# Kernel optimization log

Hardware: AMD Instinct MI355X
Metric: run time of the kernel (lower is better)

## Reference

```python
import jax, jax.numpy as jnp
import numpy as np

N_NODES = 100000
N_EDGES = 1600000
D_IN = 64
D_OUT = 64
ALPHA = 0.5


def setup_inputs() -> dict:
    key = jax.random.key(0)
    k_x, k_ei, k_w, k_ws, k_bs, k_wd, k_bd = jax.random.split(key, 7)
    x = jax.random.normal(k_x, (N_NODES, D_IN), dtype=jnp.float32)
    edge_index = jax.random.randint(k_ei, (2, N_EDGES), 0, N_NODES, dtype=jnp.int64)
    edge_weight = jax.random.uniform(k_w, (N_EDGES,), dtype=jnp.float32)
    # torch Linear init: uniform(-1/sqrt(fan_in), 1/sqrt(fan_in))
    bound = 1.0 / np.sqrt(D_IN)
    W_src = jax.random.uniform(k_ws, (D_OUT, D_IN), minval=-bound, maxval=bound, dtype=jnp.float32)
    b_src = jax.random.uniform(k_bs, (D_OUT,), minval=-bound, maxval=bound, dtype=jnp.float32)
    W_dst = jax.random.uniform(k_wd, (D_OUT, D_IN), minval=-bound, maxval=bound, dtype=jnp.float32)
    b_dst = jax.random.uniform(k_bd, (D_OUT,), minval=-bound, maxval=bound, dtype=jnp.float32)
    return {"x": x, "edge_index": edge_index, "edge_weight": edge_weight,
            "W_src": W_src, "b_src": b_src, "W_dst": W_dst, "b_dst": b_dst}


def _dir_norm_spmm(row, col, w, x, n):
    """Compute (D_out^{-1/2} A D_in^{-1/2}) @ x for A with entries (row, col, w)."""
    out_deg = jax.ops.segment_sum(w, row, num_segments=n)  # row sums (dim=1)
    in_deg = jax.ops.segment_sum(w, col, num_segments=n)   # col sums (dim=0)
    d_out = jnp.where(out_deg > 0, out_deg ** -0.5, 0.0)
    d_in = jnp.where(in_deg > 0, in_deg ** -0.5, 0.0)
    w_norm = w * d_out[row] * d_in[col]                    # [E]
    # SpMM: out[i] = sum_{e: row_e = i} w_norm_e * x[col_e]
    return jax.ops.segment_sum(w_norm[:, None] * x[col], row, num_segments=n)


def reference(x, edge_index, edge_weight, W_src, b_src, W_dst, b_dst):
    row, col = edge_index[0], edge_index[1]
    n = x.shape[0]
    agg_fwd = _dir_norm_spmm(row, col, edge_weight, x, n)   # adj_norm @ x
    agg_bwd = _dir_norm_spmm(col, row, edge_weight, x, n)   # adj_t_norm @ x
    out = ALPHA * (agg_fwd @ W_src.T + b_src) + (1.0 - ALPHA) * (agg_bwd @ W_dst.T + b_dst)
    return out
```

## Files before the change

### kernel.cpp

```cpp
#include <hip/hip_runtime.h>

#define D 64
#define ALPHA 0.5f
#define FXSCALE 16777216.f
#define CE 2048
#define BSH 9
#define BN 512

typedef unsigned long long u64;
typedef unsigned short u16;
typedef unsigned int u32;
typedef float f32x4 __attribute__((ext_vector_type(4)));

static __device__ __forceinline__ u16 f2bf(float f) {
    unsigned u = __float_as_uint(f);
    unsigned r = (u + 0x7fffu + ((u >> 16) & 1u)) >> 16;
    return (u16)r;
}
static __device__ __forceinline__ float bf2f(u16 h) {
    return __uint_as_float(((unsigned)h) << 16);
}
static __device__ __forceinline__ float dinv_of_fx(u32 fx) {
    float s = (float)fx * (1.f / FXSCALE);
    return (s > 0.f) ? rsqrtf(s) : 0.f;
}

__global__ void p1_hist_kernel(const int* __restrict__ row, const int* __restrict__ col,
                               int* __restrict__ bh, int N, int E, int NCH, int NBUCK) {
    __shared__ u32 h[512];
    int t = threadIdx.x, ch = blockIdx.x;
    h[t] = 0;
    __syncthreads();
    int e0 = ch * CE, e1 = min(E, e0 + CE);
    for (int e = e0 + t; e < e1; e += 512) {
        atomicAdd(&h[(u32)row[e] >> BSH], 1u);
        atomicAdd(&h[(u32)(N + col[e]) >> BSH], 1u);
    }
    __syncthreads();
    for (int b = t; b < NBUCK; b += 512)
        bh[(size_t)b * NCH + ch] = (int)h[b];
}

__global__ void scan1i_kernel(const int* __restrict__ src, int* __restrict__ bsum, int SZ) {
    __shared__ int s[512];
    int t = threadIdx.x;
    int i = blockIdx.x * 512 + t;
    s[t] = (i < SZ) ? src[i] : 0;
    __syncthreads();
    for (int off = 256; off; off >>= 1) {
        if (t < off) s[t] += s[t + off];
        __syncthreads();
    }
    if (t == 0) bsum[blockIdx.x] = s[0];
}

__global__ void scan2w_kernel(int* __restrict__ bsum, int nb) {
    __shared__ int s[1024];
    int t = threadIdx.x;
    int v = (t < nb) ? bsum[t] : 0;
    s[t] = v;
    __syncthreads();
    for (int off = 1; off < 1024; off <<= 1) {
        int u = (t >= off) ? s[t - off] : 0;
        __syncthreads();
        s[t] += u;
        __syncthreads();
    }
    if (t < nb) bsum[t] = s[t] - v;
}

__global__ void scan3i_kernel(const int* __restrict__ src, const int* __restrict__ bsum,
                              int* __restrict__ dst, int SZ) {
    __shared__ int s[512];
    int t = threadIdx.x;
    int i = blockIdx.x * 512 + t;
    int v = (i < SZ) ? src[i] : 0;
    s[t] = v;
    __syncthreads();
    for (int off = 1; off < 512; off <<= 1) {
        int u = (t >= off) ? s[t - off] : 0;
        __syncthreads();
        s[t] += u;
        __syncthreads();
    }
    if (i < SZ) dst[i] = bsum[blockIdx.x] + s[t] - v;
}

__global__ __launch_bounds__(512)
void p3_transform_kernel(const int* __restrict__ row, const int* __restrict__ col,
                         const float* __restrict__ w, const int* __restrict__ scanned,
                         u64* __restrict__ ent,
                         const float* __restrict__ x,
                         const float* __restrict__ Ws, const float* __restrict__ Wd,
                         u16* __restrict__ y1, u16* __restrict__ y2,
                         int N, int E, int NCH, int NBUCK, int NT, int total_blocks) {
    __shared__ u64 smem[6432];
    int b = blockIdx.x;
    int t = threadIdx.x;
    int t_before = (int)(((long long)b * NT) / total_blocks);
    bool is_t = (int)(((long long)(b + 1) * NT) / total_blocks) > t_before;

    if (!is_t) {
        int ch = b - t_before;
        u64* ebuf   = smem;
        u16* ebkt   = (u16*)(smem + 4096);
        u32* hc     = (u32*)(smem + 5120);
        u32* hstart = (u32*)(smem + 5376);
        u32* hoff   = (u32*)(smem + 5632);
        int* s      = (int*)(smem + 5888);
        hc[t] = 0;
        __syncthreads();
        int e0 = ch * CE, e1 = min(E, e0 + CE);
        for (int e = e0 + t; e < e1; e += 512) {
            atomicAdd(&hc[(u32)row[e] >> BSH], 1u);
            atomicAdd(&hc[(u32)(N + col[e]) >> BSH], 1u);
        }
        __syncthreads();
        int v = (int)hc[t];
        s[t] = v;
        __syncthreads();
        for (int off = 1; off < 512; off <<= 1) {
            int u = (t >= off) ? s[t - off] : 0;
            __syncthreads();
            s[t] += u;
            __syncthreads();
        }
        hstart[t] = (u32)(s[t] - v);
        hoff[t]   = (u32)(s[t] - v);
        hc[t] = (t < NBUCK) ? (u32)scanned[(size_t)t * NCH + ch] : 0u;
        __syncthreads();
        for (int e = e0 + t; e < e1; e += 512) {
            int r = row[e], c = col[e];
            u32 wb = __float_as_uint(w[e]);
            u32 b1 = (u32)r >> BSH;
            u64 q1 = ((u64)wb << 32) | ((u32)c << BSH) | ((u32)r & (BN - 1));
            u32 p1 = atomicAdd(&hoff[b1], 1u);
            ebuf[p1] = q1; ebkt[p1] = (u16)b1;
            u32 d2 = (u32)(N + c);
            u32 b2 = d2 >> BSH;
            u64 q2 = ((u64)wb << 32) | ((u32)r << BSH) | (d2 & (BN - 1));
            u32 p2 = atomicAdd(&hoff[b2], 1u);
            ebuf[p2] = q2; ebkt[p2] = (u16)b2;
        }
        __syncthreads();
        int nent = 2 * (e1 - e0);
        for (int p = t; p < nent; p += 512) {
            u32 bb = ebkt[p];
            ent[(size_t)hc[bb] + (u32)p - hstart[bb]] = ebuf[p];
        }
        return;
    }

    float* xs  = (float*)smem;
    float* Wt1 = xs + 64 * 65;
    float* Wt2 = Wt1 + 64 * 68;
    for (int i = t; i < 4096; i += 512) {
        int o = i >> 6, k = i & 63;
        Wt1[k * 68 + o] = Ws[i];
        Wt2[k * 68 + o] = Wd[i];
    }
    int r0 = t_before * 64;
    for (int i = t; i < 4096; i += 512) {
        int r = i >> 6, k = i & 63;
        int gr = r0 + r;
        xs[r * 65 + k] = (gr < N) ? x[(size_t)gr * D + k] : 0.f;
    }
    __syncthreads();
    int ro = t >> 4, co = t & 15;
    float a1[2][4] = {}, a2[2][4] = {};
#pragma unroll 4
    for (int k = 0; k < 64; ++k) {
        float v0 = xs[(ro * 2 + 0) * 65 + k];
        float v1 = xs[(ro * 2 + 1) * 65 + k];
        float4 b1 = *(const float4*)&Wt1[k * 68 + co * 4];
        float4 b2 = *(const float4*)&Wt2[k * 68 + co * 4];
        a1[0][0] += v0 * b1.x; a1[0][1] += v0 * b1.y; a1[0][2] += v0 * b1.z; a1[0][3] += v0 * b1.w;
        a1[1][0] += v1 * b1.x; a1[1][1] += v1 * b1.y; a1[1][2] += v1 * b1.z; a1[1][3] += v1 * b1.w;
        a2[0][0] += v0 * b2.x; a2[0][1] += v0 * b2.y; a2[0][2] += v0 * b2.z; a2[0][3] += v0 * b2.w;
        a2[1][0] += v1 * b2.x; a2[1][1] += v1 * b2.y; a2[1][2] += v1 * b2.z; a2[1][3] += v1 * b2.w;
    }
#pragma unroll
    for (int i = 0; i < 2; ++i) {
        int gr = r0 + ro * 2 + i;
        if (gr < N) {
            ushort4 o1, o2;
            o1.x = f2bf(a1[i][0] * ALPHA); o1.y = f2bf(a1[i][1] * ALPHA);
            o1.z = f2bf(a1[i][2] * ALPHA); o1.w = f2bf(a1[i][3] * ALPHA);
            o2.x = f2bf(a2[i][0] * (1.f - ALPHA)); o2.y = f2bf(a2[i][1] * (1.f - ALPHA));
            o2.z = f2bf(a2[i][2] * (1.f - ALPHA)); o2.w = f2bf(a2[i][3] * (1.f - ALPHA));
            *(ushort4*)&y1[(size_t)gr * D + co * 4] = o1;
            *(ushort4*)&y2[(size_t)gr * D + co * 4] = o2;
        }
    }
}

__global__ void p4_build_kernel(const u64* __restrict__ ent, const int* __restrict__ scanned,
                                float* __restrict__ dinv, int* __restrict__ ptr,
                                float2* __restrict__ edata,
                                int L, int NCH, int NBUCK, int total) {
    __shared__ u32 cnt[512], fx[512], pstart[512], pfill[512];
    __shared__ int s[512];
    int t = threadIdx.x, b = blockIdx.x;
    int base0 = scanned[(size_t)b * NCH];
    int base1 = (b + 1 < NBUCK) ? scanned[(size_t)(b + 1) * NCH] : total;
    int nE = base1 - base0;
    cnt[t] = 0; fx[t] = 0;
    __syncthreads();
    for (int i = t; i < nE; i += 512) {
        u64 q = ent[base0 + i];
        u32 dlo = (u32)q & (BN - 1);
        float wv = __uint_as_float((u32)(q >> 32));
        atomicAdd(&cnt[dlo], 1u);
        atomicAdd(&fx[dlo], (u32)__float2uint_rn(wv * FXSCALE));
    }
    __syncthreads();
    int v = (int)cnt[t];
    s[t] = v;
    __syncthreads();
    for (int off = 1; off < 512; off <<= 1) {
        int u = (t >= off) ? s[t - off] : 0;
        __syncthreads();
        s[t] += u;
        __syncthreads();
    }
    pstart[t] = (u32)(s[t] - v);
    pfill[t]  = (u32)(s[t] - v);
    int node = b * BN + t;
    if (node < L) {
        dinv[node] = dinv_of_fx(fx[t]);
        ptr[node] = base0 + (int)pstart[t];
    }
    if (b == 0 && t == 0) ptr[L] = total;
    __syncthreads();
    for (int i = t; i < nE; i += 512) {
        u64 q = ent[base0 + i];
        u32 dlo = (u32)q & (BN - 1);
        u32 src = ((u32)q) >> BSH;
        float wv = __uint_as_float((u32)(q >> 32));
        u32 pos = atomicAdd(&pfill[dlo], 1u);
        edata[base0 + pos] = make_float2(__int_as_float((int)src), wv);
    }
}

__global__ void gather_csr_kernel(const int* __restrict__ ptr, const float* __restrict__ dinv,
                                  const float2* __restrict__ ed,
                                  const u16* __restrict__ y1, const u16* __restrict__ y2,
                                  const float* __restrict__ b_src, const float* __restrict__ b_dst,
                                  float* __restrict__ out, int N) {
    int tid = threadIdx.x;
    int lane = tid & 63;
    int node = blockIdx.x * (blockDim.x >> 6) + (tid >> 6);
    if (node >= N) return;
    int g  = lane >> 4;
    int fl = lane & 15;

    int ef = ptr[node],     ef1 = ptr[node + 1];
    int eb = ptr[N + node], eb1 = ptr[N + node + 1];
    const float* __restrict__ dsf = dinv + N;
    const float* __restrict__ dsb = dinv;

    float f0 = 0.f, f1 = 0.f, f2 = 0.f, f3 = 0.f;
    float b0 = 0.f, b1 = 0.f, b2 = 0.f, b3 = 0.f;

    while (ef < ef1 || eb < eb1) {
        if (ef < ef1) {
            int ea = ef + g, ex = ef + 4 + g;
            float2 da = (ea < ef1) ? ed[ea] : make_float2(__int_as_float(0), 0.f);
            float2 db = (ex < ef1) ? ed[ex] : make_float2(__int_as_float(0), 0.f);
            int ea2 = ef + 8 + g, ex2 = ef + 12 + g;
            float2 dc = (ea2 < ef1) ? ed[ea2] : make_float2(__int_as_float(0), 0.f);
            float2 de = (ex2 < ef1) ? ed[ex2] : make_float2(__int_as_float(0), 0.f);
            int sa = __float_as_int(da.x), sb = __float_as_int(db.x);
            int sc = __float_as_int(dc.x), se = __float_as_int(de.x);
            float wa = da.y * dsf[sa], wb = db.y * dsf[sb];
            float wc = dc.y * dsf[sc], we = de.y * dsf[se];
            u64 qa = *(const u64*)(y1 + (((size_t)sa) << 6) + (fl << 2));
            u64 qb = *(const u64*)(y1 + (((size_t)sb) << 6) + (fl << 2));
            u64 qc = *(const u64*)(y1 + (((size_t)sc) << 6) + (fl << 2));
            u64 qe = *(const u64*)(y1 + (((size_t)se) << 6) + (fl << 2));
            f0 += wa * bf2f((u16)qa)         + wb * bf2f((u16)qb)
                + wc * bf2f((u16)qc)         + we * bf2f((u16)qe);
            f1 += wa * bf2f((u16)(qa >> 16)) + wb * bf2f((u16)(qb >> 16))
                + wc * bf2f((u16)(qc >> 16)) + we * bf2f((u16)(qe >> 16));
            f2 += wa * bf2f((u16)(qa >> 32)) + wb * bf2f((u16)(qb >> 32))
                + wc * bf2f((u16)(qc >> 32)) + we * bf2f((u16)(qe >> 32));
            f3 += wa * bf2f((u16)(qa >> 48)) + wb * bf2f((u16)(qb >> 48))
                + wc * bf2f((u16)(qc >> 48)) + we * bf2f((u16)(qe >> 48));
            ef += 16;
        }
        if (eb < eb1) {
            int ea = eb + g, ex = eb + 4 + g;
            float2 da = (ea < eb1) ? ed[ea] : make_float2(__int_as_float(0), 0.f);
            float2 db = (ex < eb1) ? ed[ex] : make_float2(__int_as_float(0), 0.f);
            int ea2 = eb + 8 + g, ex2 = eb + 12 + g;
            float2 dc = (ea2 < eb1) ? ed[ea2] : make_float2(__int_as_float(0), 0.f);
            float2 de = (ex2 < eb1) ? ed[ex2] : make_float2(__int_as_float(0), 0.f);
            int sa = __float_as_int(da.x), sb = __float_as_int(db.x);
            int sc = __float_as_int(dc.x), se = __float_as_int(de.x);
            float wa = da.y * dsb[sa], wb = db.y * dsb[sb];
            float wc = dc.y * dsb[sc], we = de.y * dsb[se];
            u64 qa = *(const u64*)(y2 + (((size_t)sa) << 6) + (fl << 2));
            u64 qb = *(const u64*)(y2 + (((size_t)sb) << 6) + (fl << 2));
            u64 qc = *(const u64*)(y2 + (((size_t)sc) << 6) + (fl << 2));
            u64 qe = *(const u64*)(y2 + (((size_t)se) << 6) + (fl << 2));
            b0 += wa * bf2f((u16)qa)         + wb * bf2f((u16)qb)
                + wc * bf2f((u16)qc)         + we * bf2f((u16)qe);
            b1 += wa * bf2f((u16)(qa >> 16)) + wb * bf2f((u16)(qb >> 16))
                + wc * bf2f((u16)(qc >> 16)) + we * bf2f((u16)(qe >> 16));
            b2 += wa * bf2f((u16)(qa >> 32)) + wb * bf2f((u16)(qb >> 32))
                + wc * bf2f((u16)(qc >> 32)) + we * bf2f((u16)(qe >> 32));
            b3 += wa * bf2f((u16)(qa >> 48)) + wb * bf2f((u16)(qb >> 48))
                + wc * bf2f((u16)(qc >> 48)) + we * bf2f((u16)(qe >> 48));
            eb += 16;
        }
    }
    float dout = dinv[node], din = dinv[N + node];
    float v0 = f0 * dout + b0 * din;
    float v1 = f1 * dout + b1 * din;
    float v2 = f2 * dout + b2 * din;
    float v3 = f3 * dout + b3 * din;
    v0 += __shfl_xor(v0, 16); v0 += __shfl_xor(v0, 32);
    v1 += __shfl_xor(v1, 16); v1 += __shfl_xor(v1, 32);
    v2 += __shfl_xor(v2, 16); v2 += __shfl_xor(v2, 32);
    v3 += __shfl_xor(v3, 16); v3 += __shfl_xor(v3, 32);
    if (g == 0) {
        float4 bs = *(const float4*)&b_src[fl << 2];
        float4 bd = *(const float4*)&b_dst[fl << 2];
        f32x4 o;
        o.x = v0 + ALPHA * bs.x + (1.f - ALPHA) * bd.x;
        o.y = v1 + ALPHA * bs.y + (1.f - ALPHA) * bd.y;
        o.z = v2 + ALPHA * bs.z + (1.f - ALPHA) * bd.z;
        o.w = v3 + ALPHA * bs.w + (1.f - ALPHA) * bd.w;
        __builtin_nontemporal_store(o, (f32x4*)&out[((size_t)node << 6) + (fl << 2)]);
    }
}

extern "C" void kernel_launch(void* const* d_in, const int* in_sizes, int n_in,
                              void* d_out, int out_size, void* d_ws, size_t ws_size,
                              hipStream_t stream) {
    const float* x     = (const float*)d_in[0];
    const int*   ei    = (const int*)d_in[1];
    const float* w     = (const float*)d_in[2];
    const float* W_src = (const float*)d_in[3];
    const float* b_src = (const float*)d_in[4];
    const float* W_dst = (const float*)d_in[5];
    const float* b_dst = (const float*)d_in[6];
    float* out = (float*)d_out;

    const int N = in_sizes[0] / D;
    const int E = in_sizes[2];
    const int* row = ei;
    const int* col = ei + E;
    const int L = 2 * N;
    const int NCH   = (E + CE - 1) / CE;
    const int NBUCK = (L + BN - 1) >> BSH;
    const int SZ    = NBUCK * NCH;
    const int NSB   = (SZ + 511) / 512;
    const int NT    = (N + 63) / 64;
    const int total = 2 * E;

    char* base = (char*)d_ws;
    size_t o = 0;
    auto take = [&](size_t b) { char* p = base + o; o = (o + b + 63) & ~(size_t)63; return p; };
    int*    bh      = (int*)take((size_t)SZ * 4);
    int*    scanned = (int*)take((size_t)SZ * 4);
    int*    bsum    = (int*)take(1024 * 4);
    u64*    ent     = (u64*)take((size_t)total * 8);
    float*  dinv    = (float*)take((size_t)L * 4);
    int*    ptr     = (int*)take((size_t)(L + 1) * 4);
    u16*    y1      = (u16*)take((size_t)N * D * 2);
    u16*    y2      = (u16*)take((size_t)N * D * 2);
    float2* edata   = (float2*)take((size_t)total * 8);

    p1_hist_kernel<<<NCH, 512, 0, stream>>>(row, col, bh, N, E, NCH, NBUCK);
    scan1i_kernel<<<NSB, 512, 0, stream>>>(bh, bsum, SZ);
    scan2w_kernel<<<1, 1024, 0, stream>>>(bsum, NSB);
    scan3i_kernel<<<NSB, 512, 0, stream>>>(bh, bsum, scanned, SZ);
    p3_transform_kernel<<<NCH + NT, 512, 0, stream>>>(row, col, w, scanned, ent,
                                                      x, W_src, W_dst, y1, y2,
                                                      N, E, NCH, NBUCK, NT, NCH + NT);
    p4_build_kernel<<<NBUCK, 512, 0, stream>>>(ent, scanned, dinv, ptr, edata,
                                               L, NCH, NBUCK, total);
    gather_csr_kernel<<<(N + 3) / 4, 256, 0, stream>>>(ptr, dinv, edata, y1, y2,
                                                       b_src, b_dst, out, N);
}
```

Before: 217.3 us.

## Replace histogram and scan kernels with per-bucket atomic cursors and fixed capacity slots

```diff
diff --git a/kernel.cpp b/kernel.cpp
--- a/kernel.cpp
+++ b/kernel.cpp
@@ -6,6 +6,7 @@
 #define CE 2048
 #define BSH 9
 #define BN 512
+#define CAP 9216
 
 typedef unsigned long long u64;
 typedef unsigned short u16;
@@ -25,70 +26,9 @@
     return (s > 0.f) ? rsqrtf(s) : 0.f;
 }
 
-__global__ void p1_hist_kernel(const int* __restrict__ row, const int* __restrict__ col,
-                               int* __restrict__ bh, int N, int E, int NCH, int NBUCK) {
-    __shared__ u32 h[512];
-    int t = threadIdx.x, ch = blockIdx.x;
-    h[t] = 0;
-    __syncthreads();
-    int e0 = ch * CE, e1 = min(E, e0 + CE);
-    for (int e = e0 + t; e < e1; e += 512) {
-        atomicAdd(&h[(u32)row[e] >> BSH], 1u);
-        atomicAdd(&h[(u32)(N + col[e]) >> BSH], 1u);
-    }
-    __syncthreads();
-    for (int b = t; b < NBUCK; b += 512)
-        bh[(size_t)b * NCH + ch] = (int)h[b];
-}
-
-__global__ void scan1i_kernel(const int* __restrict__ src, int* __restrict__ bsum, int SZ) {
-    __shared__ int s[512];
-    int t = threadIdx.x;
-    int i = blockIdx.x * 512 + t;
-    s[t] = (i < SZ) ? src[i] : 0;
-    __syncthreads();
-    for (int off = 256; off; off >>= 1) {
-        if (t < off) s[t] += s[t + off];
-        __syncthreads();
-    }
-    if (t == 0) bsum[blockIdx.x] = s[0];
-}
-
-__global__ void scan2w_kernel(int* __restrict__ bsum, int nb) {
-    __shared__ int s[1024];
-    int t = threadIdx.x;
-    int v = (t < nb) ? bsum[t] : 0;
-    s[t] = v;
-    __syncthreads();
-    for (int off = 1; off < 1024; off <<= 1) {
-        int u = (t >= off) ? s[t - off] : 0;
-        __syncthreads();
-        s[t] += u;
-        __syncthreads();
-    }
-    if (t < nb) bsum[t] = s[t] - v;
-}
-
-__global__ void scan3i_kernel(const int* __restrict__ src, const int* __restrict__ bsum,
-                              int* __restrict__ dst, int SZ) {
-    __shared__ int s[512];
-    int t = threadIdx.x;
-    int i = blockIdx.x * 512 + t;
-    int v = (i < SZ) ? src[i] : 0;
-    s[t] = v;
-    __syncthreads();
-    for (int off = 1; off < 512; off <<= 1) {
-        int u = (t >= off) ? s[t - off] : 0;
-        __syncthreads();
-        s[t] += u;
-        __syncthreads();
-    }
-    if (i < SZ) dst[i] = bsum[blockIdx.x] + s[t] - v;
-}
-
 __global__ __launch_bounds__(512)
 void p3_transform_kernel(const int* __restrict__ row, const int* __restrict__ col,
-                         const float* __restrict__ w, const int* __restrict__ scanned,
+                         const float* __restrict__ w, u32* __restrict__ cursor,
                          u64* __restrict__ ent,
                          const float* __restrict__ x,
                          const float* __restrict__ Ws, const float* __restrict__ Wd,
@@ -104,19 +44,20 @@
         int ch = b - t_before;
         u64* ebuf   = smem;
         u16* ebkt   = (u16*)(smem + 4096);
-        u32* hc     = (u32*)(smem + 5120);
+        u32* hcnt   = (u32*)(smem + 5120);
         u32* hstart = (u32*)(smem + 5376);
         u32* hoff   = (u32*)(smem + 5632);
         int* s      = (int*)(smem + 5888);
-        hc[t] = 0;
+        u32* hbase  = (u32*)(smem + 6144);
+        hcnt[t] = 0;
         __syncthreads();
         int e0 = ch * CE, e1 = min(E, e0 + CE);
         for (int e = e0 + t; e < e1; e += 512) {
-            atomicAdd(&hc[(u32)row[e] >> BSH], 1u);
-            atomicAdd(&hc[(u32)(N + col[e]) >> BSH], 1u);
-        }
-        __syncthreads();
-        int v = (int)hc[t];
+            atomicAdd(&hcnt[(u32)row[e] >> BSH], 1u);
+            atomicAdd(&hcnt[(u32)(N + col[e]) >> BSH], 1u);
+        }
+        __syncthreads();
+        int v = (int)hcnt[t];
         s[t] = v;
         __syncthreads();
         for (int off = 1; off < 512; off <<= 1) {
@@ -127,7 +68,9 @@
         }
         hstart[t] = (u32)(s[t] - v);
         hoff[t]   = (u32)(s[t] - v);
-        hc[t] = (t < NBUCK) ? (u32)scanned[(size_t)t * NCH + ch] : 0u;
+        u32 myb = 0;
+        if (t < NBUCK && v > 0) myb = atomicAdd(&cursor[t], (u32)v);
+        hbase[t] = myb;
         __syncthreads();
         for (int e = e0 + t; e < e1; e += 512) {
             int r = row[e], c = col[e];
@@ -146,7 +89,9 @@
         int nent = 2 * (e1 - e0);
         for (int p = t; p < nent; p += 512) {
             u32 bb = ebkt[p];
-            ent[(size_t)hc[bb] + (u32)p - hstart[bb]] = ebuf[p];
+            u32 local = hbase[bb] + (u32)p - hstart[bb];
+            if (local < CAP)
+                ent[(size_t)bb * CAP + local] = ebuf[p];
         }
         return;
     }
@@ -194,20 +139,19 @@
     }
 }
 
-__global__ void p4_build_kernel(const u64* __restrict__ ent, const int* __restrict__ scanned,
-                                float* __restrict__ dinv, int* __restrict__ ptr,
+__global__ void p4_build_kernel(const u64* __restrict__ ent, const u32* __restrict__ cursor,
+                                float* __restrict__ dinv, int2* __restrict__ ptr2,
                                 float2* __restrict__ edata,
-                                int L, int NCH, int NBUCK, int total) {
+                                int L, int NBUCK) {
     __shared__ u32 cnt[512], fx[512], pstart[512], pfill[512];
     __shared__ int s[512];
     int t = threadIdx.x, b = blockIdx.x;
-    int base0 = scanned[(size_t)b * NCH];
-    int base1 = (b + 1 < NBUCK) ? scanned[(size_t)(b + 1) * NCH] : total;
-    int nE = base1 - base0;
+    int base0 = b * CAP;
+    int nE = min((int)cursor[b], CAP);
     cnt[t] = 0; fx[t] = 0;
     __syncthreads();
     for (int i = t; i < nE; i += 512) {
-        u64 q = ent[base0 + i];
+        u64 q = ent[(size_t)base0 + i];
         u32 dlo = (u32)q & (BN - 1);
         float wv = __uint_as_float((u32)(q >> 32));
         atomicAdd(&cnt[dlo], 1u);
@@ -228,21 +172,21 @@
     int node = b * BN + t;
     if (node < L) {
         dinv[node] = dinv_of_fx(fx[t]);
-        ptr[node] = base0 + (int)pstart[t];
-    }
-    if (b == 0 && t == 0) ptr[L] = total;
+        int st = base0 + (int)pstart[t];
+        ptr2[node] = make_int2(st, st + v);
+    }
     __syncthreads();
     for (int i = t; i < nE; i += 512) {
-        u64 q = ent[base0 + i];
+        u64 q = ent[(size_t)base0 + i];
         u32 dlo = (u32)q & (BN - 1);
         u32 src = ((u32)q) >> BSH;
         float wv = __uint_as_float((u32)(q >> 32));
         u32 pos = atomicAdd(&pfill[dlo], 1u);
-        edata[base0 + pos] = make_float2(__int_as_float((int)src), wv);
-    }
-}
-
-__global__ void gather_csr_kernel(const int* __restrict__ ptr, const float* __restrict__ dinv,
+        edata[(size_t)base0 + pos] = make_float2(__int_as_float((int)src), wv);
+    }
+}
+
+__global__ void gather_csr_kernel(const int2* __restrict__ ptr2, const float* __restrict__ dinv,
                                   const float2* __restrict__ ed,
                                   const u16* __restrict__ y1, const u16* __restrict__ y2,
                                   const float* __restrict__ b_src, const float* __restrict__ b_dst,
@@ -254,8 +198,10 @@
     int g  = lane >> 4;
     int fl = lane & 15;
 
-    int ef = ptr[node],     ef1 = ptr[node + 1];
-    int eb = ptr[N + node], eb1 = ptr[N + node + 1];
+    int2 pf = ptr2[node];
+    int2 pb = ptr2[N + node];
+    int ef = pf.x, ef1 = pf.y;
+    int eb = pb.x, eb1 = pb.y;
     const float* __restrict__ dsf = dinv + N;
     const float* __restrict__ dsb = dinv;
 
@@ -264,10 +210,9 @@
 
     while (ef < ef1 || eb < eb1) {
         if (ef < ef1) {
-            int ea = ef + g, ex = ef + 4 + g;
-            float2 da = (ea < ef1) ? ed[ea] : make_float2(__int_as_float(0), 0.f);
-            float2 db = (ex < ef1) ? ed[ex] : make_float2(__int_as_float(0), 0.f);
-            int ea2 = ef + 8 + g, ex2 = ef + 12 + g;
+            int ea = ef + g, ex = ef + 4 + g, ea2 = ef + 8 + g, ex2 = ef + 12 + g;
+            float2 da = (ea  < ef1) ? ed[ea]  : make_float2(__int_as_float(0), 0.f);
+            float2 db = (ex  < ef1) ? ed[ex]  : make_float2(__int_as_float(0), 0.f);
             float2 dc = (ea2 < ef1) ? ed[ea2] : make_float2(__int_as_float(0), 0.f);
             float2 de = (ex2 < ef1) ? ed[ex2] : make_float2(__int_as_float(0), 0.f);
             int sa = __float_as_int(da.x), sb = __float_as_int(db.x);
@@ -289,10 +234,9 @@
             ef += 16;
         }
         if (eb < eb1) {
-            int ea = eb + g, ex = eb + 4 + g;
-            float2 da = (ea < eb1) ? ed[ea] : make_float2(__int_as_float(0), 0.f);
-            float2 db = (ex < eb1) ? ed[ex] : make_float2(__int_as_float(0), 0.f);
-            int ea2 = eb + 8 + g, ex2 = eb + 12 + g;
+            int ea = eb + g, ex = eb + 4 + g, ea2 = eb + 8 + g, ex2 = eb + 12 + g;
+            float2 da = (ea  < eb1) ? ed[ea]  : make_float2(__int_as_float(0), 0.f);
+            float2 db = (ex  < eb1) ? ed[ex]  : make_float2(__int_as_float(0), 0.f);
             float2 dc = (ea2 < eb1) ? ed[ea2] : make_float2(__int_as_float(0), 0.f);
             float2 de = (ex2 < eb1) ? ed[ex2] : make_float2(__int_as_float(0), 0.f);
             int sa = __float_as_int(da.x), sb = __float_as_int(db.x);
@@ -354,33 +298,24 @@
     const int L = 2 * N;
     const int NCH   = (E + CE - 1) / CE;
     const int NBUCK = (L + BN - 1) >> BSH;
-    const int SZ    = NBUCK * NCH;
-    const int NSB   = (SZ + 511) / 512;
     const int NT    = (N + 63) / 64;
-    const int total = 2 * E;
 
     char* base = (char*)d_ws;
     size_t o = 0;
     auto take = [&](size_t b) { char* p = base + o; o = (o + b + 63) & ~(size_t)63; return p; };
-    int*    bh      = (int*)take((size_t)SZ * 4);
-    int*    scanned = (int*)take((size_t)SZ * 4);
-    int*    bsum    = (int*)take(1024 * 4);
-    u64*    ent     = (u64*)take((size_t)total * 8);
-    float*  dinv    = (float*)take((size_t)L * 4);
-    int*    ptr     = (int*)take((size_t)(L + 1) * 4);
-    u16*    y1      = (u16*)take((size_t)N * D * 2);
-    u16*    y2      = (u16*)take((size_t)N * D * 2);
-    float2* edata   = (float2*)take((size_t)total * 8);
-
-    p1_hist_kernel<<<NCH, 512, 0, stream>>>(row, col, bh, N, E, NCH, NBUCK);
-    scan1i_kernel<<<NSB, 512, 0, stream>>>(bh, bsum, SZ);
-    scan2w_kernel<<<1, 1024, 0, stream>>>(bsum, NSB);
-    scan3i_kernel<<<NSB, 512, 0, stream>>>(bh, bsum, scanned, SZ);
-    p3_transform_kernel<<<NCH + NT, 512, 0, stream>>>(row, col, w, scanned, ent,
+    u32*    cursor = (u32*)take((size_t)NBUCK * 4);
+    u64*    ent    = (u64*)take((size_t)NBUCK * CAP * 8);
+    float*  dinv   = (float*)take((size_t)L * 4);
+    int2*   ptr2   = (int2*)take((size_t)L * 8);
+    u16*    y1     = (u16*)take((size_t)N * D * 2);
+    u16*    y2     = (u16*)take((size_t)N * D * 2);
+    float2* edata  = (float2*)take((size_t)NBUCK * CAP * 8);
+
+    hipMemsetAsync(cursor, 0, (size_t)NBUCK * 4, stream);
+    p3_transform_kernel<<<NCH + NT, 512, 0, stream>>>(row, col, w, cursor, ent,
                                                       x, W_src, W_dst, y1, y2,
                                                       N, E, NCH, NBUCK, NT, NCH + NT);
-    p4_build_kernel<<<NBUCK, 512, 0, stream>>>(ent, scanned, dinv, ptr, edata,
-                                               L, NCH, NBUCK, total);
-    gather_csr_kernel<<<(N + 3) / 4, 256, 0, stream>>>(ptr, dinv, edata, y1, y2,
+    p4_build_kernel<<<NBUCK, 512, 0, stream>>>(ent, cursor, dinv, ptr2, edata, L, NBUCK);
+    gather_csr_kernel<<<(N + 3) / 4, 256, 0, stream>>>(ptr2, dinv, edata, y1, y2,
                                                        b_src, b_dst, out, N);
 }
```

After: 203.9 us. 1.07x faster.
